# Kernel optimization log

Measured on AMD Instinct MI355X. Metric: run time of the kernel, lower is better.

## Reference

```python
import jax, jax.numpy as jnp
import numpy as np
import math

N_HEADS = 8
EMBED = 128
HEAD_DEPTH = EMBED // N_HEADS
CLIP = 10.0
NEG_INF = 1.0e10
SCALE = math.sqrt(HEAD_DEPTH)


def setup_inputs() -> dict:
    key = jax.random.key(0)
    ks = jax.random.split(key, 8)
    B, C, N = 32, 2, 512
    Q = jax.random.normal(ks[0], (B, C, N, EMBED), dtype=jnp.float32)
    K = jax.random.normal(ks[1], (B, C, N, EMBED), dtype=jnp.float32)
    V = jax.random.normal(ks[2], (B, C, N, EMBED), dtype=jnp.float32)
    mask = jax.random.bernoulli(ks[3], 0.15, (B, C, N, 1))  # True = masked out
    stdv_qkv = 1.0 / math.sqrt(HEAD_DEPTH)
    stdv_out = 1.0 / math.sqrt(EMBED)
    # torch nn.Linear weights: (out_features, in_features)
    Wq = jax.random.uniform(ks[4], (EMBED, EMBED), jnp.float32, -stdv_qkv, stdv_qkv)
    Wk = jax.random.uniform(ks[5], (EMBED, EMBED), jnp.float32, -stdv_qkv, stdv_qkv)
    Wv = jax.random.uniform(ks[6], (EMBED, EMBED), jnp.float32, -stdv_qkv, stdv_qkv)
    Wout = jax.random.uniform(ks[7], (EMBED, EMBED), jnp.float32, -stdv_out, stdv_out)
    return {"Q": Q, "K": K, "V": V, "mask": mask,
            "Wq": Wq, "Wk": Wk, "Wv": Wv, "Wout": Wout}


def _split_heads(T):
    # (b, c, n, E) -> (b, H, c, n, d)
    b, c, n, _ = T.shape
    return T.reshape(b, c, n, N_HEADS, HEAD_DEPTH).transpose(0, 3, 1, 2, 4)


def reference(Q, K, V, mask, Wq, Wk, Wv, Wout):
    # Linear projections (torch Linear: y = x @ W.T)
    q = _split_heads(jnp.einsum('bcne,fe->bcnf', Q, Wq))
    k = _split_heads(jnp.einsum('bcne,fe->bcnf', K, Wk))
    v = _split_heads(jnp.einsum('bcne,fe->bcnf', V, Wv))
    # logits: (b, H, c, q, k)
    logits = jnp.einsum('bhcqd,bhckd->bhcqk', q, k) / SCALE
    logits = CLIP * jnp.tanh(logits)
    # mask (b, c, n, 1) -> (b, 1, c, 1, n); True -> -1e10
    m = mask[:, None, :, :, :].swapaxes(-1, -2)
    logits = jnp.where(m, -NEG_INF, logits)
    probs = jax.nn.softmax(logits, axis=-1)
    out = jnp.einsum('bhcqk,bhckd->bhcqd', probs, v)
    # combine heads: (b, H, c, n, d) -> (b, c, n, E)
    b, h, c, n, d = out.shape
    out = out.transpose(0, 2, 3, 1, 4).reshape(b, c, n, EMBED)
    return jnp.einsum('bcne,fe->bcnf', out, Wout)
```

## Files before the change

### kernel.cpp

```cpp
#include <hip/hip_runtime.h>

typedef _Float16 half_t;
typedef _Float16 half8 __attribute__((ext_vector_type(8)));
typedef _Float16 half4 __attribute__((ext_vector_type(4)));
typedef float floatx4 __attribute__((ext_vector_type(4)));
typedef float floatx16 __attribute__((ext_vector_type(16)));

#define C1 0.72134752044448170368f
#define C2 14.4269504088896340736f
#define C3 28.8539008177792681472f

__device__ __forceinline__ floatx4 zero4() {
    floatx4 z; z[0] = z[1] = z[2] = z[3] = 0.f; return z;
}
__device__ __forceinline__ floatx16 zero16() {
    floatx16 z;
#pragma unroll
    for (int i = 0; i < 16; ++i) z[i] = 0.f;
    return z;
}

__device__ __forceinline__ float pfun(float sp, float b) {
    float u = __builtin_amdgcn_exp2f(sp);
    float r = __builtin_amdgcn_rcpf(u + 1.0f);
    return __builtin_amdgcn_exp2f(b - C3 * r);
}

__global__ void k_convw(const float* __restrict__ Wq, const float* __restrict__ Wk,
                        const float* __restrict__ Wv, const float* __restrict__ Wo,
                        half_t* __restrict__ Wh) {
    int idx = blockIdx.x * 256 + threadIdx.x;
    int which = idx >> 14;
    int off = idx & 16383;
    const float* src = (which == 0) ? Wq : (which == 1) ? Wk : (which == 2) ? Wv : Wo;
    float scale = (which == 0) ? C1 : 1.0f;
    Wh[idx] = (half_t)(src[off] * scale);
}

__global__ __launch_bounds__(256) void k_proj(
        const float* __restrict__ Q, const float* __restrict__ K,
        const float* __restrict__ V, const half_t* __restrict__ WhBase,
        half_t* __restrict__ qw, half_t* __restrict__ kw, half_t* __restrict__ vw) {
    int which = blockIdx.y;
    const float* X = (which == 0) ? Q : (which == 1) ? K : V;
    const half_t* W = WhBase + which * 16384;

    int tid = threadIdx.x;
    int w = tid >> 6, lane = tid & 63;
    int l15 = lane & 15, quad = lane >> 4;
    int tokbase = blockIdx.x * 64 + w * 16;

    floatx4 acc[8];
#pragma unroll
    for (int nt = 0; nt < 8; ++nt) acc[nt] = zero4();

#pragma unroll
    for (int ks = 0; ks < 4; ++ks) {
        const float* ap = X + (tokbase + l15) * 128 + ks * 32 + quad * 8;
        float4 a0 = *(const float4*)ap;
        float4 a1 = *(const float4*)(ap + 4);
        half8 xf;
        xf[0] = (half_t)a0.x; xf[1] = (half_t)a0.y; xf[2] = (half_t)a0.z; xf[3] = (half_t)a0.w;
        xf[4] = (half_t)a1.x; xf[5] = (half_t)a1.y; xf[6] = (half_t)a1.z; xf[7] = (half_t)a1.w;
        if (which == 2) {
#pragma unroll
            for (int nt = 0; nt < 8; ++nt) {
                half8 wf = *(const half8*)(W + (nt * 16 + l15) * 128 + ks * 32 + quad * 8);
                acc[nt] = __builtin_amdgcn_mfma_f32_16x16x32_f16(xf, wf, acc[nt], 0, 0, 0);
            }
        } else {
#pragma unroll
            for (int nt = 0; nt < 8; ++nt) {
                half8 wf = *(const half8*)(W + (nt * 16 + l15) * 128 + ks * 32 + quad * 8);
                acc[nt] = __builtin_amdgcn_mfma_f32_16x16x32_f16(wf, xf, acc[nt], 0, 0, 0);
            }
        }
    }

    if (which == 2) {
        int R0 = tokbase + quad * 4;
        int bc = R0 >> 9, n0 = R0 & 511;
#pragma unroll
        for (int nt = 0; nt < 8; ++nt) {
            half4 hv;
            hv[0] = (half_t)acc[nt][0]; hv[1] = (half_t)acc[nt][1];
            hv[2] = (half_t)acc[nt][2]; hv[3] = (half_t)acc[nt][3];
            *(half4*)(vw + ((bc * 8 + nt) * 16 + l15) * 512 + n0) = hv;
        }
    } else {
        int R = tokbase + l15;
        int bc = R >> 9, n = R & 511;
        half_t* Y = (which == 0) ? qw : kw;
#pragma unroll
        for (int nt = 0; nt < 8; ++nt) {
            half4 hv;
            hv[0] = (half_t)acc[nt][0]; hv[1] = (half_t)acc[nt][1];
            hv[2] = (half_t)acc[nt][2]; hv[3] = (half_t)acc[nt][3];
            *(half4*)(Y + ((bc * 8 + nt) * 512 + n) * 16 + quad * 4) = hv;
        }
    }
}

__global__ __launch_bounds__(256, 8) void k_attn(
        const half_t* __restrict__ qg, const half_t* __restrict__ kg,
        const half_t* __restrict__ vTg, const int* __restrict__ mask,
        half_t* __restrict__ attn) {
    __shared__ float bias[512];
    __shared__ half_t Pl[4][32 * 36];

    int bx = blockIdx.x;
    int bch = bx >> 2, qq = bx & 3;
    int bc = bch >> 3, h = bch & 7;
    int tid = threadIdx.x;
    int w = tid >> 6, lane = tid & 63;
    int l31 = lane & 31, hf = lane >> 5;
    int l15 = lane & 15, quad = lane >> 4;

    const half_t* qh = qg + bch * 8192;
    const half_t* kh = kg + bch * 8192;
    const half_t* vh = vTg + bch * 8192;

    for (int i = tid; i < 512; i += 256)
        bias[i] = mask[bc * 512 + i] ? -1.0e30f : C2;
    __syncthreads();

    int qbase = qq * 128 + w * 32;
    half8 qf = *(const half8*)(qh + (qbase + l31) * 16 + hf * 8);

    floatx4 O[2];
    O[0] = zero4(); O[1] = zero4();
    float rs = 0.f;
    half_t* Pw = &Pl[w][0];
    const float4* b4 = (const float4*)bias;

#pragma unroll 1
    for (int c = 0; c < 16; ++c) {
        half8 kf = *(const half8*)(kh + (c * 32 + l31) * 16 + hf * 8);
        half8 vf = *(const half8*)(vh + l15 * 512 + c * 32 + quad * 8);
        float4 bv[4];
#pragma unroll
        for (int g = 0; g < 4; ++g) bv[g] = b4[c * 8 + hf + 2 * g];

        floatx16 S = __builtin_amdgcn_mfma_f32_32x32x16_f16(kf, qf, zero16(), 0, 0, 0);
        float rsum = 0.f;
#pragma unroll
        for (int g = 0; g < 4; ++g) {
            float p0 = pfun(S[4 * g + 0], bv[g].x);
            float p1 = pfun(S[4 * g + 1], bv[g].y);
            float p2 = pfun(S[4 * g + 2], bv[g].z);
            float p3 = pfun(S[4 * g + 3], bv[g].w);
            rsum += (p0 + p1) + (p2 + p3);
            half4 ph;
            ph[0] = (half_t)p0; ph[1] = (half_t)p1;
            ph[2] = (half_t)p2; ph[3] = (half_t)p3;
            *(half4*)(Pw + l31 * 36 + hf * 4 + g * 8) = ph;
        }
        rs += rsum;
#pragma unroll
        for (int nt2 = 0; nt2 < 2; ++nt2) {
            half8 pb = *(const half8*)(Pw + (nt2 * 16 + l15) * 36 + quad * 8);
            O[nt2] = __builtin_amdgcn_mfma_f32_16x16x32_f16(vf, pb, O[nt2], 0, 0, 0);
        }
    }

    float r2 = rs + __shfl_xor(rs, 32, 64);
    float inv = __builtin_amdgcn_rcpf(r2);
#pragma unroll
    for (int nt = 0; nt < 2; ++nt) {
        float iv = __shfl(inv, (nt << 4) | l15, 64);
        int qrow = qbase + nt * 16 + l15;
        half4 ov;
        ov[0] = (half_t)(O[nt][0] * iv);
        ov[1] = (half_t)(O[nt][1] * iv);
        ov[2] = (half_t)(O[nt][2] * iv);
        ov[3] = (half_t)(O[nt][3] * iv);
        *(half4*)(attn + (bc * 512 + qrow) * 128 + h * 16 + quad * 4) = ov;
    }
}

__global__ __launch_bounds__(256) void k_out(
        const half_t* __restrict__ A, const half_t* __restrict__ Wh,
        float* __restrict__ out) {
    int tid = threadIdx.x;
    int w = tid >> 6, lane = tid & 63;
    int l15 = lane & 15, quad = lane >> 4;
    int tokbase = blockIdx.x * 64 + w * 16;

    floatx4 acc[8];
#pragma unroll
    for (int nt = 0; nt < 8; ++nt) acc[nt] = zero4();
#pragma unroll
    for (int ks = 0; ks < 4; ++ks) {
        half8 xf = *(const half8*)(A + (tokbase + l15) * 128 + ks * 32 + quad * 8);
#pragma unroll
        for (int nt = 0; nt < 8; ++nt) {
            half8 wf = *(const half8*)(Wh + (nt * 16 + l15) * 128 + ks * 32 + quad * 8);
            acc[nt] = __builtin_amdgcn_mfma_f32_16x16x32_f16(wf, xf, acc[nt], 0, 0, 0);
        }
    }
#pragma unroll
    for (int nt = 0; nt < 8; ++nt) {
        float4 o;
        o.x = acc[nt][0]; o.y = acc[nt][1]; o.z = acc[nt][2]; o.w = acc[nt][3];
        *(float4*)(out + (tokbase + l15) * 128 + nt * 16 + quad * 4) = o;
    }
}

extern "C" void kernel_launch(void* const* d_in, const int* in_sizes, int n_in,
                              void* d_out, int out_size, void* d_ws, size_t ws_size,
                              hipStream_t stream) {
    const float* Q    = (const float*)d_in[0];
    const float* K    = (const float*)d_in[1];
    const float* V    = (const float*)d_in[2];
    const int*   mask = (const int*)d_in[3];
    const float* Wq   = (const float*)d_in[4];
    const float* Wk   = (const float*)d_in[5];
    const float* Wv   = (const float*)d_in[6];
    const float* Wo   = (const float*)d_in[7];
    float* out = (float*)d_out;

    half_t* ws = (half_t*)d_ws;
    half_t* Wh = ws;
    half_t* qw = ws + 65536;
    half_t* kw = qw + 4194304;
    half_t* vw = kw + 4194304;
    half_t* aw = vw + 4194304;

    k_convw<<<256, 256, 0, stream>>>(Wq, Wk, Wv, Wo, Wh);
    k_proj<<<dim3(512, 3), 256, 0, stream>>>(Q, K, V, Wh, qw, kw, vw);
    k_attn<<<2048, 256, 0, stream>>>(qw, kw, vw, mask, aw);
    k_out<<<512, 256, 0, stream>>>(aw, Wh + 49152, out);
}
```

Before: 182.3 us.

## Use single-wave attention blocks and compute row sums via MFMA with ones

The attention kernel now launches 8192 single-wavefront blocks instead of 2048 four-wave blocks, each wave handling 32 query rows with its own small LDS tile. The softmax denominator is no longer accumulated with scalar adds and a cross-lane shuffle; a second MFMA against a vector of ones produces per-row sums directly in the output layout. Probabilities are packed with cvt_pkrtz. The aim is to cut VALU work and shuffles and improve scheduling flexibility, at the cost of extra MFMA issue and each block rebuilding the 512-entry mask bias.

```diff
diff --git a/kernel.cpp b/kernel.cpp
--- a/kernel.cpp
+++ b/kernel.cpp
@@ -101,18 +101,17 @@
     }
 }
 
-__global__ __launch_bounds__(256, 8) void k_attn(
+__global__ __launch_bounds__(64, 8) void k_attn(
         const half_t* __restrict__ qg, const half_t* __restrict__ kg,
         const half_t* __restrict__ vTg, const int* __restrict__ mask,
         half_t* __restrict__ attn) {
     __shared__ float bias[512];
-    __shared__ half_t Pl[4][32 * 36];
+    __shared__ half_t Pb[32 * 36];
 
     int bx = blockIdx.x;
-    int bch = bx >> 2, qq = bx & 3;
+    int bch = bx >> 4, qt = bx & 15;
     int bc = bch >> 3, h = bch & 7;
-    int tid = threadIdx.x;
-    int w = tid >> 6, lane = tid & 63;
+    int lane = threadIdx.x;
     int l31 = lane & 31, hf = lane >> 5;
     int l15 = lane & 15, quad = lane >> 4;
 
@@ -120,17 +119,21 @@
     const half_t* kh = kg + bch * 8192;
     const half_t* vh = vTg + bch * 8192;
 
-    for (int i = tid; i < 512; i += 256)
-        bias[i] = mask[bc * 512 + i] ? -1.0e30f : C2;
+#pragma unroll
+    for (int i = 0; i < 8; ++i)
+        bias[i * 64 + lane] = mask[bc * 512 + i * 64 + lane] ? -1.0e30f : C2;
     __syncthreads();
 
-    int qbase = qq * 128 + w * 32;
+    int qbase = qt * 32;
     half8 qf = *(const half8*)(qh + (qbase + l31) * 16 + hf * 8);
 
-    floatx4 O[2];
+    half8 ones;
+#pragma unroll
+    for (int j = 0; j < 8; ++j) ones[j] = (half_t)1.0f;
+
+    floatx4 O[2], Os[2];
     O[0] = zero4(); O[1] = zero4();
-    float rs = 0.f;
-    half_t* Pw = &Pl[w][0];
+    Os[0] = zero4(); Os[1] = zero4();
     const float4* b4 = (const float4*)bias;
 
 #pragma unroll 1
@@ -142,32 +145,30 @@
         for (int g = 0; g < 4; ++g) bv[g] = b4[c * 8 + hf + 2 * g];
 
         floatx16 S = __builtin_amdgcn_mfma_f32_32x32x16_f16(kf, qf, zero16(), 0, 0, 0);
-        float rsum = 0.f;
 #pragma unroll
         for (int g = 0; g < 4; ++g) {
             float p0 = pfun(S[4 * g + 0], bv[g].x);
             float p1 = pfun(S[4 * g + 1], bv[g].y);
             float p2 = pfun(S[4 * g + 2], bv[g].z);
             float p3 = pfun(S[4 * g + 3], bv[g].w);
-            rsum += (p0 + p1) + (p2 + p3);
+            auto t0 = __builtin_amdgcn_cvt_pkrtz(p0, p1);
+            auto t1 = __builtin_amdgcn_cvt_pkrtz(p2, p3);
             half4 ph;
-            ph[0] = (half_t)p0; ph[1] = (half_t)p1;
-            ph[2] = (half_t)p2; ph[3] = (half_t)p3;
-            *(half4*)(Pw + l31 * 36 + hf * 4 + g * 8) = ph;
-        }
-        rs += rsum;
+            ph[0] = (half_t)t0[0]; ph[1] = (half_t)t0[1];
+            ph[2] = (half_t)t1[0]; ph[3] = (half_t)t1[1];
+            *(half4*)(Pb + l31 * 36 + hf * 4 + g * 8) = ph;
+        }
 #pragma unroll
         for (int nt2 = 0; nt2 < 2; ++nt2) {
-            half8 pb = *(const half8*)(Pw + (nt2 * 16 + l15) * 36 + quad * 8);
-            O[nt2] = __builtin_amdgcn_mfma_f32_16x16x32_f16(vf, pb, O[nt2], 0, 0, 0);
-        }
-    }
-
-    float r2 = rs + __shfl_xor(rs, 32, 64);
-    float inv = __builtin_amdgcn_rcpf(r2);
+            half8 pb = *(const half8*)(Pb + (nt2 * 16 + l15) * 36 + quad * 8);
+            O[nt2]  = __builtin_amdgcn_mfma_f32_16x16x32_f16(vf,   pb, O[nt2],  0, 0, 0);
+            Os[nt2] = __builtin_amdgcn_mfma_f32_16x16x32_f16(ones, pb, Os[nt2], 0, 0, 0);
+        }
+    }
+
 #pragma unroll
     for (int nt = 0; nt < 2; ++nt) {
-        float iv = __shfl(inv, (nt << 4) | l15, 64);
+        float iv = __builtin_amdgcn_rcpf(Os[nt][0]);
         int qrow = qbase + nt * 16 + l15;
         half4 ov;
         ov[0] = (half_t)(O[nt][0] * iv);
@@ -228,6 +229,6 @@
 
     k_convw<<<256, 256, 0, stream>>>(Wq, Wk, Wv, Wo, Wh);
     k_proj<<<dim3(512, 3), 256, 0, stream>>>(Q, K, V, Wh, qw, kw, vw);
-    k_attn<<<2048, 256, 0, stream>>>(qw, kw, vw, mask, aw);
+    k_attn<<<8192, 64, 0, stream>>>(qw, kw, vw, mask, aw);
     k_out<<<512, 256, 0, stream>>>(aw, Wh + 49152, out);
 }
```

After: 180.1 us. About the same (-1.2%).
